# Optimization experiments

Measured on AMD Instinct MI355X. Metric: run time of the kernel, lower is better.

## Reference

```python
import jax, jax.numpy as jnp
import numpy as np

N_USER = 50000
N_ITEM = 100000
N = N_USER + N_ITEM
NNZ = 3_000_000
EMB = 64
BATCH = 4096


def _l2norm(x, eps=1e-12):
    # torch F.normalize(p=2, dim=1): x / max(||x||, eps)
    n = jnp.sqrt(jnp.sum(x * x, axis=1, keepdims=True))
    return x / jnp.maximum(n, eps)


def setup_inputs() -> dict:
    key = jax.random.key(0)
    ks = jax.random.split(key, 12)
    users = jax.random.randint(ks[0], (BATCH,), 0, N_USER, dtype=jnp.int64 if jax.config.jax_enable_x64 else jnp.int32)
    rows = jax.random.randint(ks[1], (NNZ,), 0, N, dtype=jnp.int32)
    cols = jax.random.randint(ks[2], (NNZ,), 0, N, dtype=jnp.int32)
    vals = jax.random.uniform(ks[3], (NNZ,), dtype=jnp.float32)
    user_emb = jax.random.normal(ks[4], (N_USER, EMB), dtype=jnp.float32) * 0.1
    item_emb = jax.random.normal(ks[5], (N_ITEM, EMB), dtype=jnp.float32) * 0.1
    W0 = jax.random.normal(ks[6], (EMB, EMB), dtype=jnp.float32) * 0.1
    b0 = jax.random.normal(ks[7], (1, EMB), dtype=jnp.float32) * 0.1
    W1 = jax.random.normal(ks[8], (EMB, EMB), dtype=jnp.float32) * 0.1
    b1 = jax.random.normal(ks[9], (1, EMB), dtype=jnp.float32) * 0.1
    W2 = jax.random.normal(ks[10], (EMB, EMB), dtype=jnp.float32) * 0.1
    b2 = jax.random.normal(ks[11], (1, EMB), dtype=jnp.float32) * 0.1
    return {"users": users, "rows": rows, "cols": cols, "vals": vals,
            "user_emb": user_emb, "item_emb": item_emb,
            "W0": W0, "b0": b0, "W1": W1, "b1": b1, "W2": W2, "b2": b2}


def reference(users, rows, cols, vals, user_emb, item_emb, W0, b0, W1, b1, W2, b2):
    ego = jnp.concatenate([user_emb, item_emb], axis=0)  # [N, EMB]
    total = ego  # all_embeddings[0]
    for W, b in ((W0, b0), (W1, b1), (W2, b2)):
        # SpMM: side[r] = sum_e vals[e] * ego[cols[e]] for rows[e]==r
        side = jax.ops.segment_sum(vals[:, None] * ego[cols], rows, num_segments=N)
        ego = jax.nn.leaky_relu(side @ W + b, negative_slope=0.2)
        total = total + _l2norm(ego)
    u_g = total[:N_USER]
    return u_g[users]  # [BATCH, EMB]
```

## Files before the change

kernel.cpp:

```cpp
#include <hip/hip_runtime.h>
#include <hip/hip_fp16.h>

#define N_USER 50000
#define N_ITEM 100000
#define NTOT   150000
#define NNZ    3000000
#define EMB    64
#define BATCH  4096

#define BROWS  128
#define NB     1172
#define BCAP   3008
#define CHUNK  6144
#define NBUCK  489
#define EGO4   (NTOT * EMB / 4)
#define EGOB   2344
#define OUTB   ((BATCH * EMB) / 1024)

typedef unsigned short u16;
typedef unsigned int   u32;
typedef unsigned long long u64;
typedef _Float16 f16;
typedef f16   f16x8 __attribute__((ext_vector_type(8)));
typedef float f32x4 __attribute__((ext_vector_type(4)));

__device__ __forceinline__ void scan_excl(const int* src, int* dst, int* wsum,
                                          int tid, int lane, int w) {
    int carry = 0;
    for (int base = 0; base < NB; base += 1024) {
        int i = base + tid;
        int x = (i < NB) ? src[i] : 0;
        int v = x;
#pragma unroll
        for (int off = 1; off < 64; off <<= 1) {
            int y = __shfl_up(v, off);
            if (lane >= off) v += y;
        }
        if (lane == 63) wsum[w] = v;
        __syncthreads();
        if (tid < 16) {
            int s = wsum[tid];
#pragma unroll
            for (int off = 1; off < 16; off <<= 1) {
                int y = __shfl_up(s, off);
                if (tid >= off) s += y;
            }
            wsum[tid] = s;
        }
        __syncthreads();
        int excl = carry + (w ? wsum[w - 1] : 0) + v - x;
        if (i < NB) dst[i] = excl;
        carry += wsum[15];
        __syncthreads();
    }
}

__global__ __launch_bounds__(1024) void k_prep(const int* __restrict__ rows,
                                               const int* __restrict__ cols,
                                               const float* __restrict__ vals,
                                               int* __restrict__ bcnt,
                                               int2* __restrict__ bbuf,
                                               const float4* __restrict__ ue4,
                                               const float4* __restrict__ ie4,
                                               uint2* __restrict__ ego,
                                               const float* __restrict__ ue,
                                               const int* __restrict__ users,
                                               float* __restrict__ out) {
    int bi = blockIdx.x, tid = threadIdx.x;
    if (bi >= NBUCK) {
        int bj = bi - NBUCK;
        if (bj < EGOB) {
            int i = bj * 1024 + tid;
            if (i < EGO4) {
                const int UF4 = N_USER * EMB / 4;
                float4 f = (i < UF4) ? ue4[i] : ie4[i - UF4];
                __half2 h0 = __floats2half2_rn(f.x, f.y);
                __half2 h1 = __floats2half2_rn(f.z, f.w);
                ego[i] = make_uint2(*(u32*)&h0, *(u32*)&h1);
            }
        } else {
            int t = (bj - EGOB) * 1024 + tid;
            int w = t >> 6, lane = t & 63;
            int u = users[w];
            out[w * EMB + lane] = ue[(size_t)u * EMB + lane];
        }
        return;
    }

    __shared__ int2 stage[CHUNK];
    __shared__ u16  sbuck[CHUNK];
    __shared__ int  hist[NB], cur[NB], gbase[NB];
    __shared__ int  wsum[16];
    int lane = tid & 63, w = tid >> 6;
    int start = bi * CHUNK;
    int n = min(start + CHUNK, NNZ) - start;

    for (int i = tid; i < NB; i += 1024) hist[i] = 0;
    __syncthreads();

    u32 ex[6], ev[6];
    int eb[6];
#pragma unroll
    for (int u = 0; u < 6; ++u) {
        int i = u * 1024 + tid;
        if (i < n) {
            int e = start + i;
            int r = rows[e];
            ex[u] = (u32)cols[e] | ((u32)(r & 127) << 18);
            ev[u] = (u32)__float_as_int(vals[e]);
            eb[u] = r >> 7;
            atomicAdd(&hist[eb[u]], 1);
        }
    }
    __syncthreads();

    for (int i = tid; i < NB; i += 1024) {
        int h = hist[i];
        gbase[i] = h ? atomicAdd(&bcnt[i * 16], h) : 0;
    }
    scan_excl(hist, cur, wsum, tid, lane, w);

#pragma unroll
    for (int u = 0; u < 6; ++u) {
        int i = u * 1024 + tid;
        if (i < n) {
            int pos = atomicAdd(&cur[eb[u]], 1);
            stage[pos] = make_int2((int)ex[u], (int)ev[u]);
            sbuck[pos] = (u16)eb[u];
        }
    }
    __syncthreads();
    for (int j = tid; j < n; j += 1024) {
        int b = sbuck[j];
        int pos = gbase[b] + (j - (cur[b] - hist[b]));
        if (pos < BCAP)
            bbuf[(size_t)b * BCAP + pos] = stage[j];
    }
}

__global__ __launch_bounds__(512) void k_fused(const int* __restrict__ bcnt,
                                               const int2* __restrict__ bbuf,
                                               const f16* __restrict__ ego_in,
                                               const float* __restrict__ W,
                                               const float* __restrict__ bias,
                                               u16* __restrict__ ego_out) {
    __shared__ __align__(16) char ubuf[BCAP * 8];
    __shared__ f16  Wl[64 * 72];
    __shared__ int  hist[128], cur[128], rowptr[129];
    __shared__ int  ws2[2];
    int2* stg = (int2*)ubuf;
    f16*  S16 = (f16*)ubuf;
    int tid = threadIdx.x, lane = tid & 63, w = tid >> 6;

    int b = blockIdx.x;
    int cnt = min(bcnt[b * 16], BCAP);
    const int2* src = bbuf + (size_t)b * BCAP;

    for (int i = tid; i < 4096; i += 512) {
        int k = i >> 6, n = i & 63;
        Wl[n * 72 + k] = (f16)W[i];
    }
    if (tid < 128) hist[tid] = 0;
    __syncthreads();

    u32 fx[6], fv[6];
#pragma unroll
    for (int u = 0; u < 6; ++u) {
        int i = u * 512 + tid;
        if (i < cnt) {
            int2 e = src[i];
            fx[u] = (u32)e.x;
            fv[u] = (u32)e.y;
            atomicAdd(&hist[(fx[u] >> 18) & 127], 1);
        }
    }
    __syncthreads();

    int sx = 0, sv = 0;
    if (tid < 128) {
        sx = hist[tid]; sv = sx;
#pragma unroll
        for (int off = 1; off < 64; off <<= 1) {
            int y = __shfl_up(sv, off);
            if (lane >= off) sv += y;
        }
        if (lane == 63) ws2[tid >> 6] = sv;
    }
    __syncthreads();
    if (tid < 128) {
        int excl = sv - sx + ((tid >= 64) ? ws2[0] : 0);
        rowptr[tid] = excl;
        cur[tid]    = excl;
    }
    if (tid == 0) rowptr[128] = cnt;
    __syncthreads();

#pragma unroll
    for (int u = 0; u < 6; ++u) {
        int i = u * 512 + tid;
        if (i < cnt) {
            int pos = atomicAdd(&cur[(fx[u] >> 18) & 127], 1);
            stg[pos] = make_int2((int)fx[u], (int)fv[u]);
        }
    }
    __syncthreads();

    const char* egob = (const char*)ego_in;
    int slot = lane >> 3, d8 = lane & 7;
    int rA = w * 16 + slot;
    int rB = rA + 8;
    int eA = rowptr[rA], kA = rowptr[rA + 1];
    int eB = rowptr[rB], kB = rowptr[rB + 1];
    float accA[8], accB[8];
#pragma unroll
    for (int j = 0; j < 8; ++j) { accA[j] = 0.f; accB[j] = 0.f; }
    while (__any((eA < kA) || (eB < kB))) {
        bool a0 = eA < kA, a1 = (eA + 1) < kA;
        bool b0 = eB < kB, b1 = (eB + 1) < kB;
        uint4 gA0, gA1, gB0, gB1;
        float vA0 = 0.f, vA1 = 0.f, vB0 = 0.f, vB1 = 0.f;
        if (a0) {
            int2 p = stg[eA];
            gA0 = *(const uint4*)(egob + ((size_t)(p.x & 0x3FFFF) << 7) + d8 * 16);
            vA0 = __int_as_float(p.y);
        }
        if (a1) {
            int2 p = stg[eA + 1];
            gA1 = *(const uint4*)(egob + ((size_t)(p.x & 0x3FFFF) << 7) + d8 * 16);
            vA1 = __int_as_float(p.y);
        }
        if (b0) {
            int2 p = stg[eB];
            gB0 = *(const uint4*)(egob + ((size_t)(p.x & 0x3FFFF) << 7) + d8 * 16);
            vB0 = __int_as_float(p.y);
        }
        if (b1) {
            int2 p = stg[eB + 1];
            gB1 = *(const uint4*)(egob + ((size_t)(p.x & 0x3FFFF) << 7) + d8 * 16);
            vB1 = __int_as_float(p.y);
        }
        if (a0) {
            float2 f0 = __half22float2(*(const __half2*)&gA0.x);
            float2 f1 = __half22float2(*(const __half2*)&gA0.y);
            float2 f2 = __half22float2(*(const __half2*)&gA0.z);
            float2 f3 = __half22float2(*(const __half2*)&gA0.w);
            accA[0] = fmaf(vA0, f0.x, accA[0]); accA[1] = fmaf(vA0, f0.y, accA[1]);
            accA[2] = fmaf(vA0, f1.x, accA[2]); accA[3] = fmaf(vA0, f1.y, accA[3]);
            accA[4] = fmaf(vA0, f2.x, accA[4]); accA[5] = fmaf(vA0, f2.y, accA[5]);
            accA[6] = fmaf(vA0, f3.x, accA[6]); accA[7] = fmaf(vA0, f3.y, accA[7]);
        }
        if (a1) {
            float2 f0 = __half22float2(*(const __half2*)&gA1.x);
            float2 f1 = __half22float2(*(const __half2*)&gA1.y);
            float2 f2 = __half22float2(*(const __half2*)&gA1.z);
            float2 f3 = __half22float2(*(const __half2*)&gA1.w);
            accA[0] = fmaf(vA1, f0.x, accA[0]); accA[1] = fmaf(vA1, f0.y, accA[1]);
            accA[2] = fmaf(vA1, f1.x, accA[2]); accA[3] = fmaf(vA1, f1.y, accA[3]);
            accA[4] = fmaf(vA1, f2.x, accA[4]); accA[5] = fmaf(vA1, f2.y, accA[5]);
            accA[6] = fmaf(vA1, f3.x, accA[6]); accA[7] = fmaf(vA1, f3.y, accA[7]);
        }
        if (b0) {
            float2 f0 = __half22float2(*(const __half2*)&gB0.x);
            float2 f1 = __half22float2(*(const __half2*)&gB0.y);
            float2 f2 = __half22float2(*(const __half2*)&gB0.z);
            float2 f3 = __half22float2(*(const __half2*)&gB0.w);
            accB[0] = fmaf(vB0, f0.x, accB[0]); accB[1] = fmaf(vB0, f0.y, accB[1]);
            accB[2] = fmaf(vB0, f1.x, accB[2]); accB[3] = fmaf(vB0, f1.y, accB[3]);
            accB[4] = fmaf(vB0, f2.x, accB[4]); accB[5] = fmaf(vB0, f2.y, accB[5]);
            accB[6] = fmaf(vB0, f3.x, accB[6]); accB[7] = fmaf(vB0, f3.y, accB[7]);
        }
        if (b1) {
            float2 f0 = __half22float2(*(const __half2*)&gB1.x);
            float2 f1 = __half22float2(*(const __half2*)&gB1.y);
            float2 f2 = __half22float2(*(const __half2*)&gB1.z);
            float2 f3 = __half22float2(*(const __half2*)&gB1.w);
            accB[0] = fmaf(vB1, f0.x, accB[0]); accB[1] = fmaf(vB1, f0.y, accB[1]);
            accB[2] = fmaf(vB1, f1.x, accB[2]); accB[3] = fmaf(vB1, f1.y, accB[3]);
            accB[4] = fmaf(vB1, f2.x, accB[4]); accB[5] = fmaf(vB1, f2.y, accB[5]);
            accB[6] = fmaf(vB1, f3.x, accB[6]); accB[7] = fmaf(vB1, f3.y, accB[7]);
        }
        eA += 2; eB += 2;
    }
    __syncthreads();
    {
        f16x8 hA, hB;
#pragma unroll
        for (int j = 0; j < 8; ++j) { hA[j] = (f16)accA[j]; hB[j] = (f16)accB[j]; }
        *(f16x8*)&S16[rA * 72 + d8 * 8] = hA;
        *(f16x8*)&S16[rB * 72 + d8 * 8] = hB;
    }
    __syncthreads();

    int m = lane & 15, quad = lane >> 4;
    int rowbase = b * BROWS;
    int m0 = w * 16;
    f32x4 C[4] = {{0.f,0.f,0.f,0.f},{0.f,0.f,0.f,0.f},{0.f,0.f,0.f,0.f},{0.f,0.f,0.f,0.f}};
#pragma unroll
    for (int kk = 0; kk < 2; ++kk) {
        f16x8 A = *(const f16x8*)&S16[(m0 + m) * 72 + kk * 32 + quad * 8];
#pragma unroll
        for (int nt = 0; nt < 4; ++nt) {
            f16x8 B = *(const f16x8*)&Wl[(nt * 16 + m) * 72 + kk * 32 + quad * 8];
            C[nt] = __builtin_amdgcn_mfma_f32_16x16x32_f16(A, B, C[nt], 0, 0, 0);
        }
    }
#pragma unroll
    for (int nt = 0; nt < 4; ++nt) {
        float bv = bias[nt * 16 + m];
#pragma unroll
        for (int r = 0; r < 4; ++r) {
            int orow = rowbase + m0 + quad * 4 + r;
            float o = C[nt][r] + bv;
            o = o > 0.f ? o : 0.2f * o;
            if (orow < NTOT) {
                __half hh = __float2half(o);
                ego_out[(size_t)orow * EMB + nt * 16 + m] = *(u16*)&hh;
            }
        }
    }
}

__global__ __launch_bounds__(256) void k_accum(const __half* __restrict__ ego,
                                               const int* __restrict__ users,
                                               float* __restrict__ out) {
    int t = blockIdx.x * 256 + threadIdx.x;
    int w = t >> 6, lane = t & 63;
    int u = users[w];
    float x = __half2float(ego[(size_t)u * EMB + lane]);
    float ss = x * x;
#pragma unroll
    for (int off = 32; off; off >>= 1) ss += __shfl_xor(ss, off);
    float n = sqrtf(ss);
    out[w * EMB + lane] += x / fmaxf(n, 1e-12f);
}

extern "C" void kernel_launch(void* const* d_in, const int* in_sizes, int n_in,
                              void* d_out, int out_size, void* d_ws, size_t ws_size,
                              hipStream_t stream) {
    const int*   users = (const int*)d_in[0];
    const int*   rows  = (const int*)d_in[1];
    const int*   cols  = (const int*)d_in[2];
    const float* vals  = (const float*)d_in[3];
    const float* ue    = (const float*)d_in[4];
    const float* ie    = (const float*)d_in[5];
    const float* Ws[3] = {(const float*)d_in[6], (const float*)d_in[8], (const float*)d_in[10]};
    const float* bs[3] = {(const float*)d_in[7], (const float*)d_in[9], (const float*)d_in[11]};
    float* out = (float*)d_out;

    char* p = (char*)d_ws;
    f16*  egoA  = (f16*)p;  p += (size_t)NTOT * EMB * 2;
    f16*  egoB  = (f16*)p;  p += (size_t)NTOT * EMB * 2;
    int2* bbuf  = (int2*)p; p += (size_t)NB * BCAP * 8;
    int*  bcnt  = (int*)p;  p += (size_t)NB * 16 * 4;

    hipMemsetAsync(bcnt, 0, (size_t)NB * 16 * 4, stream);
    k_prep<<<NBUCK + EGOB + OUTB, 1024, 0, stream>>>(
        rows, cols, vals, bcnt, bbuf,
        (const float4*)ue, (const float4*)ie, (uint2*)egoA, ue, users, out);

    const int grids[3] = {NB, NB, (N_USER + BROWS - 1) / BROWS};
    f16* bufs[2] = {egoA, egoB};
    for (int l = 0; l < 3; ++l) {
        const f16* src = bufs[l & 1];
        f16*       dst = bufs[(l + 1) & 1];
        k_fused<<<grids[l], 512, 0, stream>>>(bcnt, bbuf, src, Ws[l], bs[l], (u16*)dst);
        k_accum<<<(BATCH * EMB) / 256, 256, 0, stream>>>((const __half*)dst, users, out);
    }
}
```

Baseline: 322.5 us.

## Compute final layer only for batch users in a dedicated gather kernel

After: 325.0 us. About the same (+0.8%).

```diff
diff --git a/kernel.cpp b/kernel.cpp
--- a/kernel.cpp
+++ b/kernel.cpp
@@ -334,6 +334,56 @@
     out[w * EMB + lane] += x / fmaxf(n, 1e-12f);
 }
 
+__global__ __launch_bounds__(512) void k_user(const int* __restrict__ bcnt,
+                                              const int2* __restrict__ bbuf,
+                                              const f16* __restrict__ ego_in,
+                                              const float* __restrict__ W,
+                                              const float* __restrict__ bias,
+                                              const int* __restrict__ users,
+                                              float* __restrict__ out) {
+    __shared__ float Wl[64 * 64];
+    int tid = threadIdx.x, lane = tid & 63, w = tid >> 6;
+    for (int i = tid; i < 4096; i += 512) Wl[i] = W[i];
+    __syncthreads();
+
+    int wid = blockIdx.x * 8 + w;
+    int u = users[wid];
+    int b = u >> 7;
+    u32 rl = (u32)(u & 127);
+    int cnt = min(bcnt[b * 16], BCAP);
+    const int2* src = bbuf + (size_t)b * BCAP;
+
+    float acc = 0.f;
+    for (int base = 0; base < cnt; base += 64) {
+        int j = base + lane;
+        int2 e = make_int2(0, 0);
+        bool valid = j < cnt;
+        if (valid) e = src[j];
+        bool m = valid && ((((u32)e.x >> 18) & 127) == rl);
+        u64 mask = __ballot(m);
+        while (mask) {
+            int sl = __ffsll((long long)mask) - 1;
+            mask &= mask - 1;
+            int col = __shfl(e.x, sl) & 0x3FFFF;
+            float v = __int_as_float(__shfl(e.y, sl));
+            acc = fmaf(v, (float)ego_in[(size_t)col * EMB + lane], acc);
+        }
+    }
+
+    float y = bias[lane];
+#pragma unroll
+    for (int k = 0; k < 64; ++k) {
+        float sk = __shfl(acc, k);
+        y = fmaf(sk, Wl[k * 64 + lane], y);
+    }
+    y = y > 0.f ? y : 0.2f * y;
+    float ss = y * y;
+#pragma unroll
+    for (int off = 32; off; off >>= 1) ss += __shfl_xor(ss, off);
+    float n = sqrtf(ss);
+    out[wid * EMB + lane] += y / fmaxf(n, 1e-12f);
+}
+
 extern "C" void kernel_launch(void* const* d_in, const int* in_sizes, int n_in,
                               void* d_out, int out_size, void* d_ws, size_t ws_size,
                               hipStream_t stream) {
@@ -358,12 +408,13 @@
         rows, cols, vals, bcnt, bbuf,
         (const float4*)ue, (const float4*)ie, (uint2*)egoA, ue, users, out);
 
-    const int grids[3] = {NB, NB, (N_USER + BROWS - 1) / BROWS};
     f16* bufs[2] = {egoA, egoB};
-    for (int l = 0; l < 3; ++l) {
+    for (int l = 0; l < 2; ++l) {
         const f16* src = bufs[l & 1];
         f16*       dst = bufs[(l + 1) & 1];
-        k_fused<<<grids[l], 512, 0, stream>>>(bcnt, bbuf, src, Ws[l], bs[l], (u16*)dst);
+        k_fused<<<NB, 512, 0, stream>>>(bcnt, bbuf, src, Ws[l], bs[l], (u16*)dst);
         k_accum<<<(BATCH * EMB) / 256, 256, 0, stream>>>((const __half*)dst, users, out);
     }
-}
+    k_user<<<BATCH / 8, 512, 0, stream>>>(bcnt, bbuf, (const f16*)egoA,
+                                          Ws[2], bs[2], users, out);
+}
```
